# Optimization experiments

Measured on AMD Instinct MI355X. Metric: run time of the kernel, lower is better.

## Reference

```python
import jax, jax.numpy as jnp
import numpy as np
from jax import lax

D_MODEL, D_INNER, D_CONV, D_STATE, DT_RANK = 1024, 2048, 4, 16, 64
B, L = 2, 1024


def setup_inputs() -> dict:
    key = jax.random.key(0)
    ks = jax.random.split(key, 10)
    s = 0.02
    return {
        "x": jax.random.normal(ks[0], (B, L, D_MODEL), jnp.float32),
        "in_proj_w": jax.random.normal(ks[1], (2 * D_INNER, D_MODEL), jnp.float32) * s,
        "conv_w": jax.random.normal(ks[2], (D_INNER, 1, D_CONV), jnp.float32) * 0.1,
        "conv_b": jax.random.normal(ks[3], (D_INNER,), jnp.float32) * s,
        "x_proj_w": jax.random.normal(ks[4], (DT_RANK + 2 * D_STATE, D_INNER), jnp.float32) * s,
        "dt_proj_w": jax.random.normal(ks[5], (D_INNER, DT_RANK), jnp.float32) * s,
        "dt_proj_b": jax.random.normal(ks[6], (D_INNER,), jnp.float32) * s,
        "A_log": jnp.log(jnp.broadcast_to(jnp.arange(1, D_STATE + 1, dtype=jnp.float32), (D_INNER, D_STATE))),
        "D": jax.random.normal(ks[7], (D_INNER,), jnp.float32),
        "out_proj_w": jax.random.normal(ks[8], (D_MODEL, D_INNER), jnp.float32) * s,
    }


def _silu(v):
    return v * jax.nn.sigmoid(v)


def reference(x, in_proj_w, conv_w, conv_b, x_proj_w, dt_proj_w, dt_proj_b, A_log, D, out_proj_w):
    # in_proj: [B,L,d_model] -> [B,L,2*d_inner], split into x and gate z
    xz = jnp.einsum("bld,ed->ble", x, in_proj_w)
    xi, z = jnp.split(xz, 2, axis=-1)  # each [B,L,d_inner]

    # depthwise causal conv1d (padding = d_conv-1 on the left, output length L)
    xc = jnp.transpose(xi, (0, 2, 1))  # [B, d_inner, L]
    xc = lax.conv_general_dilated(
        xc, conv_w, window_strides=(1,), padding=[(D_CONV - 1, 0)],
        feature_group_count=D_INNER, dimension_numbers=("NCH", "OIH", "NCH"))
    xc = xc + conv_b[None, :, None]
    xc = _silu(jnp.transpose(xc, (0, 2, 1)))  # [B,L,d_inner]

    # selective scan parameters
    x_dbl = jnp.einsum("bld,ed->ble", xc, x_proj_w)  # [B,L,dt_rank+2*d_state]
    dt, Bm, Cm = jnp.split(x_dbl, [DT_RANK, DT_RANK + D_STATE], axis=-1)
    delta = jax.nn.softplus(jnp.einsum("blr,dr->bld", dt, dt_proj_w) + dt_proj_b)  # [B,L,d_inner]
    A = -jnp.exp(A_log)  # [d_inner, d_state]

    deltaA = jnp.exp(delta[..., None] * A)                       # [B,L,d_inner,N]
    deltaBu = delta[..., None] * Bm[:, :, None, :] * xc[..., None]  # [B,L,d_inner,N]

    def step(h, inp):
        a, bu, c = inp
        h = a * h + bu                         # [B,d_inner,N]
        y = jnp.einsum("bdn,bn->bd", h, c)     # [B,d_inner]
        return h, y

    h0 = jnp.zeros((x.shape[0], D_INNER, D_STATE), xc.dtype)
    _, ys = lax.scan(step, h0, (jnp.moveaxis(deltaA, 1, 0),
                                jnp.moveaxis(deltaBu, 1, 0),
                                jnp.moveaxis(Cm, 1, 0)))
    y = jnp.moveaxis(ys, 0, 1)  # [B,L,d_inner]

    y = y + xc * D
    y = y * _silu(z)
    return jnp.einsum("bld,ed->ble", y, out_proj_w)  # [B,L,d_model]
```

## Files before the change

kernel.cpp:

```cpp
#include <hip/hip_runtime.h>
#include <math.h>
#include <stdint.h>

#define DMODEL 1024
#define DINNER 2048
#define DCONV  4
#define DSTATE 16
#define DTRANK 64
#define BB 2
#define LL 1024
#define MM (BB * LL)

#define CL  64
#define NCH (LL / CL)

#define AS1(p) ((__attribute__((address_space(1))) void*)(void*)(p))
#define AS3(p) ((__attribute__((address_space(3))) void*)(void*)(p))

typedef __attribute__((ext_vector_type(8))) short bf16x8;
typedef __attribute__((ext_vector_type(4))) float f32x4;

__device__ __forceinline__ ushort bf16_rne(float f) {
  uint32_t u = __float_as_uint(f);
  uint32_t r = (u + 0x7fffu + ((u >> 16) & 1u)) >> 16;
  return (ushort)r;
}

__device__ __forceinline__ void split4(const float* __restrict__ in,
                                       ushort* __restrict__ hi,
                                       ushort* __restrict__ lo, int i4) {
  const float4 v = *reinterpret_cast<const float4*>(in + (size_t)i4 * 4);
  ushort4 h;
  h.x = bf16_rne(v.x); h.y = bf16_rne(v.y);
  h.z = bf16_rne(v.z); h.w = bf16_rne(v.w);
  *reinterpret_cast<ushort4*>(hi + (size_t)i4 * 4) = h;
  if (lo) {
    ushort4 l;
    l.x = bf16_rne(v.x - __uint_as_float((uint)h.x << 16));
    l.y = bf16_rne(v.y - __uint_as_float((uint)h.y << 16));
    l.z = bf16_rne(v.z - __uint_as_float((uint)h.z << 16));
    l.w = bf16_rne(v.w - __uint_as_float((uint)h.w << 16));
    *reinterpret_cast<ushort4*>(lo + (size_t)i4 * 4) = l;
  }
}

__global__ __launch_bounds__(256)
void split3(const float* s0, ushort* h0, ushort* l0, int n0,
            const float* s1, ushort* h1, ushort* l1, int n1,
            const float* s2, ushort* h2, ushort* l2, int n2,
            const float* s3, ushort* h3, ushort* l3, int n3) {
  int i = blockIdx.x * 256 + threadIdx.x;
  if (i < n0) { split4(s0, h0, l0, i); return; }
  i -= n0;
  if (i < n1) { split4(s1, h1, l1, i); return; }
  i -= n1;
  if (i < n2) { split4(s2, h2, l2, i); return; }
  i -= n2;
  if (i < n3) { split4(s3, h3, l3, i); return; }
}

__device__ __forceinline__ int swz4(int r) { return (r & 3) ^ ((r >> 2) & 3); }

template<int EPI, int SPLITK>
__global__ __launch_bounds__(256)
void gemm_hl_mfma(const ushort* __restrict__ Ahg, const ushort* __restrict__ Alg,
                  const ushort* __restrict__ Bhg, const ushort* __restrict__ Blg,
                  float* __restrict__ C, const float* __restrict__ bias,
                  int M, int N, int K) {
  __shared__ ushort Ah[2][128][32];
  __shared__ ushort Al[2][128][32];
  __shared__ ushort Bh[2][128][32];
  __shared__ ushort Bl[2][128][32];

  const int tid  = threadIdx.x;
  const int wave = tid >> 6;
  const int lane = tid & 63;
  const int m0 = blockIdx.y * 128;
  const int n0 = blockIdx.x * 128;
  const int wm = (wave >> 1) * 64;
  const int wn = (wave & 1) * 64;

  const int ksl = K / SPLITK;
  const int kb  = blockIdx.z * ksl;
  float* Cout   = C + (size_t)blockIdx.z * M * N;

  f32x4 acc[4][4];
  #pragma unroll
  for (int i = 0; i < 4; ++i)
    #pragma unroll
    for (int j = 0; j < 4; ++j)
      acc[i][j] = (f32x4){0.f, 0.f, 0.f, 0.f};

  const ushort* gsrc; ushort* dst; int row0;
  if      (wave == 0) { gsrc = Ahg; dst = &Ah[0][0][0]; row0 = m0; }
  else if (wave == 1) { gsrc = Alg; dst = &Al[0][0][0]; row0 = m0; }
  else if (wave == 2) { gsrc = Bhg; dst = &Bh[0][0][0]; row0 = n0; }
  else                { gsrc = Blg; dst = &Bl[0][0][0]; row0 = n0; }

  const int lr = lane >> 2;
  const int ls = lane & 3;
  const int fr = lane & 15;
  const int q  = lane >> 4;

  auto STAGE = [&](int bi, int k0) {
    ushort* d = dst + bi * 4096;
    #pragma unroll
    for (int seg = 0; seg < 8; ++seg) {
      const int rho = seg * 16 + lr;
      const int ks  = (ls ^ swz4(rho)) * 8;
      __builtin_amdgcn_global_load_lds(
          AS1(gsrc + (size_t)(row0 + rho) * K + k0 + ks),
          AS3(d + seg * 512), 16, 0, 0);
    }
  };

  const int NT = ksl / 32;
  STAGE(0, kb);
  __syncthreads();

  int cur = 0;
  for (int kt = 0; kt < NT; ++kt) {
    if (kt + 1 < NT) STAGE(cur ^ 1, kb + (kt + 1) * 32);

    bf16x8 ah[4], al[4], bh[4], bl[4];
    #pragma unroll
    for (int f = 0; f < 4; ++f) {
      { const int r = wm + f * 16 + fr; const int s = 8 * (q ^ swz4(r));
        ah[f] = *reinterpret_cast<const bf16x8*>(&Ah[cur][r][s]);
        al[f] = *reinterpret_cast<const bf16x8*>(&Al[cur][r][s]); }
      { const int r = wn + f * 16 + fr; const int s = 8 * (q ^ swz4(r));
        bh[f] = *reinterpret_cast<const bf16x8*>(&Bh[cur][r][s]);
        bl[f] = *reinterpret_cast<const bf16x8*>(&Bl[cur][r][s]); }
    }
    #pragma unroll
    for (int i = 0; i < 4; ++i)
      #pragma unroll
      for (int j = 0; j < 4; ++j) {
        acc[i][j] = __builtin_amdgcn_mfma_f32_16x16x32_bf16(ah[i], bh[j], acc[i][j], 0, 0, 0);
        acc[i][j] = __builtin_amdgcn_mfma_f32_16x16x32_bf16(al[i], bh[j], acc[i][j], 0, 0, 0);
        acc[i][j] = __builtin_amdgcn_mfma_f32_16x16x32_bf16(ah[i], bl[j], acc[i][j], 0, 0, 0);
      }

    __syncthreads();
    cur ^= 1;
  }

  const int cr = (lane >> 4) * 4;
  const int cc = lane & 15;
  #pragma unroll
  for (int i = 0; i < 4; ++i)
    #pragma unroll
    for (int j = 0; j < 4; ++j) {
      const int cn = n0 + wn + j * 16 + cc;
      const float bj = (EPI == 1) ? bias[cn] : 0.f;
      const size_t base = (size_t)(m0 + wm + i * 16 + cr) * N + cn;
      #pragma unroll
      for (int r = 0; r < 4; ++r) {
        float v = acc[i][j][r];
        if (EPI == 1) {
          v += bj;
          v = fmaxf(v, 0.f) + __logf(1.f + __expf(-fabsf(v)));
        }
        Cout[base + (size_t)r * N] = v;
      }
    }
}

template<int EPI, int SPLITK>
__global__ __launch_bounds__(256)
void gemm_p2_mfma(const ushort* __restrict__ Ahg, const ushort* __restrict__ Bhg,
                  const ushort* __restrict__ Blg, float* __restrict__ P,
                  int M, int N, int K) {
  __shared__ ushort Ah[2][128][32];
  __shared__ ushort Bh[2][128][32];
  __shared__ ushort Bl[2][128][32];

  const int tid  = threadIdx.x;
  const int wave = tid >> 6;
  const int lane = tid & 63;
  const int m0 = blockIdx.y * 128;
  const int n0 = blockIdx.x * 128;
  const int wm = (wave >> 1) * 64;
  const int wn = (wave & 1) * 64;

  const int ksl = K / SPLITK;
  const int kb  = blockIdx.z * ksl;
  float* Cout   = P + (size_t)blockIdx.z * M * N;

  f32x4 acc[4][4];
  #pragma unroll
  for (int i = 0; i < 4; ++i)
    #pragma unroll
    for (int j = 0; j < 4; ++j)
      acc[i][j] = (f32x4){0.f, 0.f, 0.f, 0.f};

  const ushort* gsrc = nullptr; ushort* dst = nullptr; int row0 = 0;
  if      (wave == 0) { gsrc = Ahg; dst = &Ah[0][0][0]; row0 = m0; }
  else if (wave == 1) { gsrc = Bhg; dst = &Bh[0][0][0]; row0 = n0; }
  else if (wave == 2) { gsrc = Blg; dst = &Bl[0][0][0]; row0 = n0; }

  const int lr = lane >> 2;
  const int ls = lane & 3;
  const int fr = lane & 15;
  const int q  = lane >> 4;

  auto STAGE = [&](int bi, int k0) {
    if (wave >= 3) return;
    ushort* d = dst + bi * 4096;
    #pragma unroll
    for (int seg = 0; seg < 8; ++seg) {
      const int rho = seg * 16 + lr;
      const int ks  = (ls ^ swz4(rho)) * 8;
      __builtin_amdgcn_global_load_lds(
          AS1(gsrc + (size_t)(row0 + rho) * K + k0 + ks),
          AS3(d + seg * 512), 16, 0, 0);
    }
  };

  const int NT = ksl / 32;
  STAGE(0, kb);
  __syncthreads();

  int cur = 0;
  for (int kt = 0; kt < NT; ++kt) {
    if (kt + 1 < NT) STAGE(cur ^ 1, kb + (kt + 1) * 32);

    bf16x8 ah[4], bh[4], bl[4];
    #pragma unroll
    for (int f = 0; f < 4; ++f) {
      { const int r = wm + f * 16 + fr; const int s = 8 * (q ^ swz4(r));
        ah[f] = *reinterpret_cast<const bf16x8*>(&Ah[cur][r][s]); }
      { const int r = wn + f * 16 + fr; const int s = 8 * (q ^ swz4(r));
        bh[f] = *reinterpret_cast<const bf16x8*>(&Bh[cur][r][s]);
        bl[f] = *reinterpret_cast<const bf16x8*>(&Bl[cur][r][s]); }
    }
    #pragma unroll
    for (int i = 0; i < 4; ++i)
      #pragma unroll
      for (int j = 0; j < 4; ++j) {
        acc[i][j] = __builtin_amdgcn_mfma_f32_16x16x32_bf16(ah[i], bh[j], acc[i][j], 0, 0, 0);
        acc[i][j] = __builtin_amdgcn_mfma_f32_16x16x32_bf16(ah[i], bl[j], acc[i][j], 0, 0, 0);
      }

    __syncthreads();
    cur ^= 1;
  }

  const int cr = (lane >> 4) * 4;
  const int cc = lane & 15;
  #pragma unroll
  for (int i = 0; i < 4; ++i)
    #pragma unroll
    for (int j = 0; j < 4; ++j) {
      const int cn = n0 + wn + j * 16 + cc;
      const size_t base = (size_t)(m0 + wm + i * 16 + cr) * N + cn;
      #pragma unroll
      for (int r = 0; r < 4; ++r) {
        float v = acc[i][j][r];
        if (EPI == 2 && cn >= DINNER)
          v = v / (1.f + __expf(-v));
        Cout[base + (size_t)r * N] = v;
      }
    }
}

__global__ __launch_bounds__(256)
void splitk_reduce4(const float* __restrict__ P, float* __restrict__ out, int n) {
  const int i = (blockIdx.x * 256 + threadIdx.x) * 4;
  if (i >= n) return;
  float4 s = *reinterpret_cast<const float4*>(P + i);
  #pragma unroll
  for (int z = 1; z < 4; ++z) {
    const float4 v = *reinterpret_cast<const float4*>(P + (size_t)z * n + i);
    s.x += v.x; s.y += v.y; s.z += v.z; s.w += v.w;
  }
  *reinterpret_cast<float4*>(out + i) = s;
}

template<int BM, int BN, int TM, int TN, int KSLICE>
__global__ __launch_bounds__(256)
void gemm_nt_part(const float* __restrict__ A, const float* __restrict__ Bw,
                  float* __restrict__ P, int M, int N, int lda, int ldb) {
  constexpr int BK  = 16;
  constexpr int NTX = BN / TN;
  constexpr int NTY = BM / TM;
  static_assert(NTX * NTY == 256, "thread tile mismatch");
  __shared__ float As[BK][BM + 4];
  __shared__ float Bs[BK][BN + 4];

  const int tid = threadIdx.x;
  const int m0  = blockIdx.y * BM;
  const int n0  = blockIdx.x * BN;
  const int kb  = blockIdx.z * KSLICE;
  const int tx  = tid % NTX;
  const int ty  = tid / NTX;

  float acc[TM][TN] = {};

  for (int k0 = kb; k0 < kb + KSLICE; k0 += BK) {
    __syncthreads();
    for (int t = tid; t < BM * 4; t += 256) {
      const int row = t >> 2, kq = t & 3;
      const float4 v = *reinterpret_cast<const float4*>(
          A + (size_t)(m0 + row) * lda + k0 + kq * 4);
      As[kq * 4 + 0][row] = v.x;
      As[kq * 4 + 1][row] = v.y;
      As[kq * 4 + 2][row] = v.z;
      As[kq * 4 + 3][row] = v.w;
    }
    for (int t = tid; t < BN * 4; t += 256) {
      const int row = t >> 2, kq = t & 3;
      const float4 v = *reinterpret_cast<const float4*>(
          Bw + (size_t)(n0 + row) * ldb + k0 + kq * 4);
      Bs[kq * 4 + 0][row] = v.x;
      Bs[kq * 4 + 1][row] = v.y;
      Bs[kq * 4 + 2][row] = v.z;
      Bs[kq * 4 + 3][row] = v.w;
    }
    __syncthreads();
    #pragma unroll
    for (int k = 0; k < BK; ++k) {
      float a[TM], b[TN];
      #pragma unroll
      for (int i = 0; i < TM; ++i) a[i] = As[k][ty * TM + i];
      #pragma unroll
      for (int j = 0; j < TN; ++j) b[j] = Bs[k][tx * TN + j];
      #pragma unroll
      for (int i = 0; i < TM; ++i)
        #pragma unroll
        for (int j = 0; j < TN; ++j)
          acc[i][j] = fmaf(a[i], b[j], acc[i][j]);
    }
  }

  float* out = P + (size_t)blockIdx.z * M * N;
  #pragma unroll
  for (int i = 0; i < TM; ++i)
    #pragma unroll
    for (int j = 0; j < TN; ++j)
      out[(size_t)(m0 + ty * TM + i) * N + n0 + tx * TN + j] = acc[i][j];
}

__global__ __launch_bounds__(256)
void xpr_fused(const float* __restrict__ part, float* __restrict__ xdbl,
               ushort* __restrict__ dth, ushort* __restrict__ dtl) {
  const int i = blockIdx.x * 256 + threadIdx.x;
  if (i >= MM * 24) return;
  const int m  = i / 24;
  const int c4 = (i % 24) * 4;
  const size_t off = (size_t)m * 96 + c4;
  float4 s = *reinterpret_cast<const float4*>(part + off);
  #pragma unroll
  for (int z = 1; z < 8; ++z) {
    const float4 v = *reinterpret_cast<const float4*>(part + (size_t)z * MM * 96 + off);
    s.x += v.x; s.y += v.y; s.z += v.z; s.w += v.w;
  }
  if (c4 < 64) {
    ushort4 h, l;
    h.x = bf16_rne(s.x); l.x = bf16_rne(s.x - __uint_as_float((uint)h.x << 16));
    h.y = bf16_rne(s.y); l.y = bf16_rne(s.y - __uint_as_float((uint)h.y << 16));
    h.z = bf16_rne(s.z); l.z = bf16_rne(s.z - __uint_as_float((uint)h.z << 16));
    h.w = bf16_rne(s.w); l.w = bf16_rne(s.w - __uint_as_float((uint)h.w << 16));
    *reinterpret_cast<ushort4*>(dth + (size_t)m * 64 + c4) = h;
    *reinterpret_cast<ushort4*>(dtl + (size_t)m * 64 + c4) = l;
  } else {
    *reinterpret_cast<float4*>(xdbl + off) = s;
  }
}

__global__ __launch_bounds__(256)
void conv_silu(const float* __restrict__ xz, const float* __restrict__ cw,
               const float* __restrict__ cb, float* __restrict__ xc) {
  const int idx = blockIdx.x * 256 + threadIdx.x;
  if (idx >= MM * DINNER / 4) return;
  const int d4 = (idx & 511) * 4;
  const int m  = idx >> 9;
  const int l  = m & (LL - 1);
  const int b  = m >> 10;

  float4 w0 = *reinterpret_cast<const float4*>(cw + (size_t)(d4 + 0) * 4);
  float4 w1 = *reinterpret_cast<const float4*>(cw + (size_t)(d4 + 1) * 4);
  float4 w2 = *reinterpret_cast<const float4*>(cw + (size_t)(d4 + 2) * 4);
  float4 w3 = *reinterpret_cast<const float4*>(cw + (size_t)(d4 + 3) * 4);
  float4 acc = *reinterpret_cast<const float4*>(cb + d4);

  #pragma unroll
  for (int j = 0; j < DCONV; ++j) {
    const int ll = l - (DCONV - 1) + j;
    if (ll >= 0) {
      const float4 xv = *reinterpret_cast<const float4*>(
          xz + ((size_t)(b * LL + ll) << 12) + d4);
      acc.x = fmaf(xv.x, (&w0.x)[j], acc.x);
      acc.y = fmaf(xv.y, (&w1.x)[j], acc.y);
      acc.z = fmaf(xv.z, (&w2.x)[j], acc.z);
      acc.w = fmaf(xv.w, (&w3.x)[j], acc.w);
    }
  }
  float4 o;
  o.x = acc.x / (1.f + __expf(-acc.x));
  o.y = acc.y / (1.f + __expf(-acc.y));
  o.z = acc.z / (1.f + __expf(-acc.z));
  o.w = acc.w / (1.f + __expf(-acc.w));
  *reinterpret_cast<float4*>(xc + (size_t)m * DINNER + d4) = o;
}

__device__ __forceinline__ void stage_tile(const float* g, int stride,
                                           float* ldst, int lane) {
  const int r  = lane >> 2;
  const int q4 = (lane & 3) * 4;
  #pragma unroll
  for (int i = 0; i < 4; ++i) {
    __builtin_amdgcn_global_load_lds(
        AS1(g + (size_t)(i * 16 + r) * stride + q4),
        AS3(ldst + i * 256), 16, 0, 0);
  }
}

__device__ __forceinline__ float quad_sum(float v) {
  int i = __float_as_int(v);
  v += __int_as_float(__builtin_amdgcn_update_dpp(0, i, 0xB1, 0xf, 0xf, true));
  i = __float_as_int(v);
  v += __int_as_float(__builtin_amdgcn_update_dpp(0, i, 0x4E, 0xf, 0xf, true));
  return v;
}

__global__ __launch_bounds__(64)
void scan_chunk_state(const float* __restrict__ delta, const float* __restrict__ xc,
                      const float* __restrict__ xdbl, const float* __restrict__ A_log,
                      float* __restrict__ hend, float* __restrict__ aprod) {
  __shared__ float dT[CL][16];
  __shared__ float xT[CL][16];
  __shared__ float bT[CL][16];

  const int idx = blockIdx.x;
  const int c  = idx & 15;
  const int dg = (idx >> 4) & 127;
  const int b  = idx >> 11;
  const int t  = threadIdx.x;
  const int ch = t >> 2;
  const int q  = t & 3;
  const int d  = dg * 16 + ch;

  const size_t r0 = (size_t)b * LL + (size_t)c * CL;
  stage_tile(delta + r0 * DINNER + dg * 16, DINNER, &dT[0][0], t);
  stage_tile(xc    + r0 * DINNER + dg * 16, DINNER, &xT[0][0], t);
  stage_tile(xdbl  + r0 * 96 + DTRANK,          96, &bT[0][0], t);

  float Adn[4];
  #pragma unroll
  for (int j = 0; j < 4; ++j)
    Adn[j] = -__expf(A_log[d * DSTATE + 4 * q + j]);
  float h0 = 0.f, h1 = 0.f, h2 = 0.f, h3 = 0.f;
  float p0 = 1.f, p1 = 1.f, p2 = 1.f, p3 = 1.f;

  __syncthreads();

  #pragma unroll 8
  for (int l = 0; l < CL; ++l) {
    const float dv = dT[l][ch];
    const float xv = xT[l][ch];
    const float4 B4 = *reinterpret_cast<const float4*>(&bT[l][4 * q]);
    const float dvx = dv * xv;
    const float a0 = __expf(dv * Adn[0]);
    const float a1 = __expf(dv * Adn[1]);
    const float a2 = __expf(dv * Adn[2]);
    const float a3 = __expf(dv * Adn[3]);
    h0 = fmaf(a0, h0, dvx * B4.x);  p0 *= a0;
    h1 = fmaf(a1, h1, dvx * B4.y);  p1 *= a1;
    h2 = fmaf(a2, h2, dvx * B4.z);  p2 *= a2;
    h3 = fmaf(a3, h3, dvx * B4.w);  p3 *= a3;
  }

  const size_t base = (((size_t)(b * NCH + c) * DINNER) + d) * DSTATE + 4 * q;
  *reinterpret_cast<float4*>(hend  + base) = (float4){h0, h1, h2, h3};
  *reinterpret_cast<float4*>(aprod + base) = (float4){p0, p1, p2, p3};
}

__global__ __launch_bounds__(256)
void scan_combine(const float* __restrict__ hend, const float* __restrict__ aprod,
                  float* __restrict__ hin) {
  const int tid = blockIdx.x * 256 + threadIdx.x;
  const size_t cstride = (size_t)DINNER * DSTATE;
  const size_t base = (size_t)(tid >> 15) * NCH * cstride + (tid & 32767);
  float h = 0.f;
  hin[base] = 0.f;
  #pragma unroll
  for (int c = 0; c < NCH - 1; ++c) {
    h = fmaf(aprod[base + (size_t)c * cstride], h, hend[base + (size_t)c * cstride]);
    hin[base + (size_t)(c + 1) * cstride] = h;
  }
}

__global__ __launch_bounds__(64)
void scan_apply(const float* __restrict__ delta, const float* __restrict__ xc,
                const float* __restrict__ xdbl, const float* __restrict__ xz,
                const float* __restrict__ A_log, const float* __restrict__ Dp,
                const float* __restrict__ hin, ushort* __restrict__ yh) {
  __shared__ float dT[CL][16];
  __shared__ float xT[CL][16];
  __shared__ float bT[CL][16];
  __shared__ float cT[CL][16];
  __shared__ float zT[CL][16];

  const int idx = blockIdx.x;
  const int c  = idx & 15;
  const int dg = (idx >> 4) & 127;
  const int b  = idx >> 11;
  const int t  = threadIdx.x;
  const int ch = t >> 2;
  const int q  = t & 3;
  const int d  = dg * 16 + ch;

  const size_t r0 = (size_t)b * LL + (size_t)c * CL;
  stage_tile(delta + r0 * DINNER + dg * 16, DINNER, &dT[0][0], t);
  stage_tile(xc    + r0 * DINNER + dg * 16, DINNER, &xT[0][0], t);
  stage_tile(xdbl  + r0 * 96 + DTRANK,          96, &bT[0][0], t);
  stage_tile(xdbl  + r0 * 96 + DTRANK + DSTATE, 96, &cT[0][0], t);
  stage_tile(xz    + (r0 << 12) + DINNER + dg * 16, 4096, &zT[0][0], t);

  float Adn[4];
  #pragma unroll
  for (int j = 0; j < 4; ++j)
    Adn[j] = -__expf(A_log[d * DSTATE + 4 * q + j]);
  const float Dd = Dp[d];

  const size_t base = (((size_t)(b * NCH + c) * DINNER) + d) * DSTATE + 4 * q;
  const float4 h4 = *reinterpret_cast<const float4*>(hin + base);
  float h0 = h4.x, h1 = h4.y, h2 = h4.z, h3 = h4.w;

  __syncthreads();

  #pragma unroll 8
  for (int l = 0; l < CL; ++l) {
    const float dv = dT[l][ch];
    const float xv = xT[l][ch];
    const float4 B4 = *reinterpret_cast<const float4*>(&bT[l][4 * q]);
    const float4 C4 = *reinterpret_cast<const float4*>(&cT[l][4 * q]);
    const float dvx = dv * xv;
    const float a0 = __expf(dv * Adn[0]);
    const float a1 = __expf(dv * Adn[1]);
    const float a2 = __expf(dv * Adn[2]);
    const float a3 = __expf(dv * Adn[3]);
    h0 = fmaf(a0, h0, dvx * B4.x);
    h1 = fmaf(a1, h1, dvx * B4.y);
    h2 = fmaf(a2, h2, dvx * B4.z);
    h3 = fmaf(a3, h3, dvx * B4.w);
    float ys = fmaf(h0, C4.x, fmaf(h1, C4.y, fmaf(h2, C4.z, h3 * C4.w)));
    ys = quad_sum(ys);
    if (q == 0) {
      const float g = zT[l][ch];
      const float tv = (ys + xv * Dd) * g;
      yh[(r0 + l) * (size_t)DINNER + d] = bf16_rne(tv);
    }
  }
}

extern "C" void kernel_launch(void* const* d_in, const int* in_sizes, int n_in,
                              void* d_out, int out_size, void* d_ws, size_t ws_size,
                              hipStream_t stream) {
  const float* x         = (const float*)d_in[0];
  const float* in_proj_w = (const float*)d_in[1];
  const float* conv_w    = (const float*)d_in[2];
  const float* conv_b    = (const float*)d_in[3];
  const float* x_proj_w  = (const float*)d_in[4];
  const float* dt_proj_w = (const float*)d_in[5];
  const float* dt_proj_b = (const float*)d_in[6];
  const float* A_log     = (const float*)d_in[7];
  const float* Dv        = (const float*)d_in[8];
  const float* out_proj_w= (const float*)d_in[9];
  float* out = (float*)d_out;

  float* ws    = (float*)d_ws;
  float* xz    = ws;
  float* xc    = xz    + (size_t)MM * 4096;
  float* xdbl  = xc    + (size_t)MM * DINNER;
  float* delta = xdbl  + (size_t)MM * 96;
  ushort* us   = (ushort*)(delta + (size_t)MM * DINNER);
  ushort* yhp  = us;
  ushort* ylp  = yhp + (size_t)MM * DINNER;
  ushort* xh   = ylp + (size_t)MM * DINNER;
  ushort* xl   = xh  + (size_t)MM * DMODEL;
  ushort* wih  = xl  + (size_t)MM * DMODEL;
  ushort* wil  = wih + (size_t)4096 * DMODEL;
  ushort* woh  = wil + (size_t)4096 * DMODEL;
  ushort* wol  = woh + (size_t)DMODEL * DINNER;

  ushort* dth = ylp;
  ushort* dtl = ylp + 131072;
  ushort* wdh = ylp + 262144;
  ushort* wdl = ylp + 393216;

  float* hend  = (float*)wih;
  float* aprod = hend  + (size_t)BB * NCH * DINNER * DSTATE;
  float* hin   = aprod + (size_t)BB * NCH * DINNER * DSTATE;
  float* part  = hend;
  float* opart = xz;

  const dim3 blk(256);

  {
    const int n0 = (MM * DMODEL) / 4, n1 = (4096 * DMODEL) / 4,
              n2 = (DMODEL * DINNER) / 4, n3 = (DINNER * DTRANK) / 4;
    split3<<<dim3((n0 + n1 + n2 + n3) / 256), blk, 0, stream>>>(
        x, xh, nullptr, n0, in_proj_w, wih, wil, n1,
        out_proj_w, woh, wol, n2, dt_proj_w, wdh, wdl, n3);
  }

  gemm_p2_mfma<2,1><<<dim3(4096 / 128, MM / 128), blk, 0, stream>>>(
      xh, wih, wil, xz, MM, 4096, DMODEL);

  conv_silu<<<dim3((MM * DINNER / 4) / 256), blk, 0, stream>>>(xz, conv_w, conv_b, xc);

  gemm_nt_part<64,32,4,2,256><<<dim3(96/32, MM/64, 8), blk, 0, stream>>>(
      xc, x_proj_w, part, MM, 96, DINNER, DINNER);
  xpr_fused<<<dim3((MM * 24 + 255) / 256), blk, 0, stream>>>(part, xdbl, dth, dtl);

  gemm_hl_mfma<1,1><<<dim3(DINNER / 128, MM / 128), blk, 0, stream>>>(
      dth, dtl, wdh, wdl, delta, dt_proj_b, MM, DINNER, DTRANK);

  scan_chunk_state<<<dim3(BB * 128 * NCH), dim3(64), 0, stream>>>(
      delta, xc, xdbl, A_log, hend, aprod);
  scan_combine<<<dim3(BB * DINNER * DSTATE / 256), blk, 0, stream>>>(
      hend, aprod, hin);
  scan_apply<<<dim3(BB * 128 * NCH), dim3(64), 0, stream>>>(
      delta, xc, xdbl, xz, A_log, Dv, hin, yhp);

  gemm_p2_mfma<0,4><<<dim3(DMODEL / 128, MM / 128, 4), blk, 0, stream>>>(
      yhp, woh, wol, opart, MM, DMODEL, DINNER);
  splitk_reduce4<<<dim3((MM * DMODEL) / 1024), blk, 0, stream>>>(
      opart, out, MM * DMODEL);
}
```

Before: 183.1 us.

## Load GEMM A operand directly to registers and drop lo-split for out_proj

Unifies the three MFMA GEMM kernels into one templated kernel that stages only the B (weight) operand through LDS and loads A fragments directly from global memory into registers, prefetching the next tile. All four waves now share the B staging work. The out_proj GEMM also drops the low bf16 correction term of its weights (NB=1), halving its MFMA count and weight traffic. This cuts LDS footprint and traffic, but A loads become uncoalesced 16-byte global reads per lane. Dropping the weight low part lowers out_proj precision.

Measured after the change: 198.6 us. +8.5%, slower.

```diff
diff --git a/kernel.cpp b/kernel.cpp
--- a/kernel.cpp
+++ b/kernel.cpp
@@ -61,16 +61,13 @@
 
 __device__ __forceinline__ int swz4(int r) { return (r & 3) ^ ((r >> 2) & 3); }
 
-template<int EPI, int SPLITK>
-__global__ __launch_bounds__(256)
-void gemm_hl_mfma(const ushort* __restrict__ Ahg, const ushort* __restrict__ Alg,
+template<int NB, bool ALO, int EPI, int SPLITK>
+__global__ __launch_bounds__(256)
+void gemm_adirect(const ushort* __restrict__ Ag, const ushort* __restrict__ Alg,
                   const ushort* __restrict__ Bhg, const ushort* __restrict__ Blg,
                   float* __restrict__ C, const float* __restrict__ bias,
                   int M, int N, int K) {
-  __shared__ ushort Ah[2][128][32];
-  __shared__ ushort Al[2][128][32];
-  __shared__ ushort Bh[2][128][32];
-  __shared__ ushort Bl[2][128][32];
+  __shared__ ushort Bst[NB * 2][128][32];
 
   const int tid  = threadIdx.x;
   const int wave = tid >> 6;
@@ -91,57 +88,75 @@
     for (int j = 0; j < 4; ++j)
       acc[i][j] = (f32x4){0.f, 0.f, 0.f, 0.f};
 
-  const ushort* gsrc; ushort* dst; int row0;
-  if      (wave == 0) { gsrc = Ahg; dst = &Ah[0][0][0]; row0 = m0; }
-  else if (wave == 1) { gsrc = Alg; dst = &Al[0][0][0]; row0 = m0; }
-  else if (wave == 2) { gsrc = Bhg; dst = &Bh[0][0][0]; row0 = n0; }
-  else                { gsrc = Blg; dst = &Bl[0][0][0]; row0 = n0; }
-
   const int lr = lane >> 2;
   const int ls = lane & 3;
   const int fr = lane & 15;
   const int q  = lane >> 4;
 
   auto STAGE = [&](int bi, int k0) {
-    ushort* d = dst + bi * 4096;
-    #pragma unroll
-    for (int seg = 0; seg < 8; ++seg) {
+    #pragma unroll
+    for (int j = 0; j < NB * 2; ++j) {
+      const int g   = wave * NB * 2 + j;
+      const int p   = g >> 3;
+      const int seg = g & 7;
+      const ushort* src = p ? Blg : Bhg;
       const int rho = seg * 16 + lr;
       const int ks  = (ls ^ swz4(rho)) * 8;
       __builtin_amdgcn_global_load_lds(
-          AS1(gsrc + (size_t)(row0 + rho) * K + k0 + ks),
-          AS3(d + seg * 512), 16, 0, 0);
+          AS1(src + (size_t)(n0 + rho) * K + k0 + ks),
+          AS3(&Bst[p * 2 + bi][0][0] + seg * 512), 16, 0, 0);
     }
   };
 
+  auto LOADA = [&](bf16x8* dh, bf16x8* dl, int kt) {
+    #pragma unroll
+    for (int f = 0; f < 4; ++f) {
+      const size_t off = (size_t)(m0 + wm + f * 16 + fr) * K + kb + kt * 32 + q * 8;
+      dh[f] = *reinterpret_cast<const bf16x8*>(Ag + off);
+      if constexpr (ALO)
+        dl[f] = *reinterpret_cast<const bf16x8*>(Alg + off);
+    }
+  };
+
   const int NT = ksl / 32;
+  bf16x8 ahc[4], alc[4], ahn[4], aln[4];
   STAGE(0, kb);
+  LOADA(ahc, alc, 0);
   __syncthreads();
 
   int cur = 0;
   for (int kt = 0; kt < NT; ++kt) {
-    if (kt + 1 < NT) STAGE(cur ^ 1, kb + (kt + 1) * 32);
-
-    bf16x8 ah[4], al[4], bh[4], bl[4];
+    if (kt + 1 < NT) {
+      STAGE(cur ^ 1, kb + (kt + 1) * 32);
+      LOADA(ahn, aln, kt + 1);
+    }
+
+    bf16x8 bh[4], bl[4];
     #pragma unroll
     for (int f = 0; f < 4; ++f) {
-      { const int r = wm + f * 16 + fr; const int s = 8 * (q ^ swz4(r));
-        ah[f] = *reinterpret_cast<const bf16x8*>(&Ah[cur][r][s]);
-        al[f] = *reinterpret_cast<const bf16x8*>(&Al[cur][r][s]); }
-      { const int r = wn + f * 16 + fr; const int s = 8 * (q ^ swz4(r));
-        bh[f] = *reinterpret_cast<const bf16x8*>(&Bh[cur][r][s]);
-        bl[f] = *reinterpret_cast<const bf16x8*>(&Bl[cur][r][s]); }
+      const int r = wn + f * 16 + fr;
+      const int s = 8 * (q ^ swz4(r));
+      bh[f] = *reinterpret_cast<const bf16x8*>(&Bst[cur][r][s]);
+      if (NB == 2)
+        bl[f] = *reinterpret_cast<const bf16x8*>(&Bst[2 + cur][r][s]);
     }
     #pragma unroll
     for (int i = 0; i < 4; ++i)
       #pragma unroll
       for (int j = 0; j < 4; ++j) {
-        acc[i][j] = __builtin_amdgcn_mfma_f32_16x16x32_bf16(ah[i], bh[j], acc[i][j], 0, 0, 0);
-        acc[i][j] = __builtin_amdgcn_mfma_f32_16x16x32_bf16(al[i], bh[j], acc[i][j], 0, 0, 0);
-        acc[i][j] = __builtin_amdgcn_mfma_f32_16x16x32_bf16(ah[i], bl[j], acc[i][j], 0, 0, 0);
+        acc[i][j] = __builtin_amdgcn_mfma_f32_16x16x32_bf16(ahc[i], bh[j], acc[i][j], 0, 0, 0);
+        if (NB == 2)
+          acc[i][j] = __builtin_amdgcn_mfma_f32_16x16x32_bf16(ahc[i], bl[j], acc[i][j], 0, 0, 0);
+        if constexpr (ALO)
+          acc[i][j] = __builtin_amdgcn_mfma_f32_16x16x32_bf16(alc[i], bh[j], acc[i][j], 0, 0, 0);
       }
 
     __syncthreads();
+    #pragma unroll
+    for (int f = 0; f < 4; ++f) {
+      ahc[f] = ahn[f];
+      if constexpr (ALO) alc[f] = aln[f];
+    }
     cur ^= 1;
   }
 
@@ -161,102 +176,6 @@
           v += bj;
           v = fmaxf(v, 0.f) + __logf(1.f + __expf(-fabsf(v)));
         }
-        Cout[base + (size_t)r * N] = v;
-      }
-    }
-}
-
-template<int EPI, int SPLITK>
-__global__ __launch_bounds__(256)
-void gemm_p2_mfma(const ushort* __restrict__ Ahg, const ushort* __restrict__ Bhg,
-                  const ushort* __restrict__ Blg, float* __restrict__ P,
-                  int M, int N, int K) {
-  __shared__ ushort Ah[2][128][32];
-  __shared__ ushort Bh[2][128][32];
-  __shared__ ushort Bl[2][128][32];
-
-  const int tid  = threadIdx.x;
-  const int wave = tid >> 6;
-  const int lane = tid & 63;
-  const int m0 = blockIdx.y * 128;
-  const int n0 = blockIdx.x * 128;
-  const int wm = (wave >> 1) * 64;
-  const int wn = (wave & 1) * 64;
-
-  const int ksl = K / SPLITK;
-  const int kb  = blockIdx.z * ksl;
-  float* Cout   = P + (size_t)blockIdx.z * M * N;
-
-  f32x4 acc[4][4];
-  #pragma unroll
-  for (int i = 0; i < 4; ++i)
-    #pragma unroll
-    for (int j = 0; j < 4; ++j)
-      acc[i][j] = (f32x4){0.f, 0.f, 0.f, 0.f};
-
-  const ushort* gsrc = nullptr; ushort* dst = nullptr; int row0 = 0;
-  if      (wave == 0) { gsrc = Ahg; dst = &Ah[0][0][0]; row0 = m0; }
-  else if (wave == 1) { gsrc = Bhg; dst = &Bh[0][0][0]; row0 = n0; }
-  else if (wave == 2) { gsrc = Blg; dst = &Bl[0][0][0]; row0 = n0; }
-
-  const int lr = lane >> 2;
-  const int ls = lane & 3;
-  const int fr = lane & 15;
-  const int q  = lane >> 4;
-
-  auto STAGE = [&](int bi, int k0) {
-    if (wave >= 3) return;
-    ushort* d = dst + bi * 4096;
-    #pragma unroll
-    for (int seg = 0; seg < 8; ++seg) {
-      const int rho = seg * 16 + lr;
-      const int ks  = (ls ^ swz4(rho)) * 8;
-      __builtin_amdgcn_global_load_lds(
-          AS1(gsrc + (size_t)(row0 + rho) * K + k0 + ks),
-          AS3(d + seg * 512), 16, 0, 0);
-    }
-  };
-
-  const int NT = ksl / 32;
-  STAGE(0, kb);
-  __syncthreads();
-
-  int cur = 0;
-  for (int kt = 0; kt < NT; ++kt) {
-    if (kt + 1 < NT) STAGE(cur ^ 1, kb + (kt + 1) * 32);
-
-    bf16x8 ah[4], bh[4], bl[4];
-    #pragma unroll
-    for (int f = 0; f < 4; ++f) {
-      { const int r = wm + f * 16 + fr; const int s = 8 * (q ^ swz4(r));
-        ah[f] = *reinterpret_cast<const bf16x8*>(&Ah[cur][r][s]); }
-      { const int r = wn + f * 16 + fr; const int s = 8 * (q ^ swz4(r));
-        bh[f] = *reinterpret_cast<const bf16x8*>(&Bh[cur][r][s]);
-        bl[f] = *reinterpret_cast<const bf16x8*>(&Bl[cur][r][s]); }
-    }
-    #pragma unroll
-    for (int i = 0; i < 4; ++i)
-      #pragma unroll
-      for (int j = 0; j < 4; ++j) {
-        acc[i][j] = __builtin_amdgcn_mfma_f32_16x16x32_bf16(ah[i], bh[j], acc[i][j], 0, 0, 0);
-        acc[i][j] = __builtin_amdgcn_mfma_f32_16x16x32_bf16(ah[i], bl[j], acc[i][j], 0, 0, 0);
-      }
-
-    __syncthreads();
-    cur ^= 1;
-  }
-
-  const int cr = (lane >> 4) * 4;
-  const int cc = lane & 15;
-  #pragma unroll
-  for (int i = 0; i < 4; ++i)
-    #pragma unroll
-    for (int j = 0; j < 4; ++j) {
-      const int cn = n0 + wn + j * 16 + cc;
-      const size_t base = (size_t)(m0 + wm + i * 16 + cr) * N + cn;
-      #pragma unroll
-      for (int r = 0; r < 4; ++r) {
-        float v = acc[i][j][r];
         if (EPI == 2 && cn >= DINNER)
           v = v / (1.f + __expf(-v));
         Cout[base + (size_t)r * N] = v;
@@ -603,11 +522,11 @@
               n2 = (DMODEL * DINNER) / 4, n3 = (DINNER * DTRANK) / 4;
     split3<<<dim3((n0 + n1 + n2 + n3) / 256), blk, 0, stream>>>(
         x, xh, nullptr, n0, in_proj_w, wih, wil, n1,
-        out_proj_w, woh, wol, n2, dt_proj_w, wdh, wdl, n3);
-  }
-
-  gemm_p2_mfma<2,1><<<dim3(4096 / 128, MM / 128), blk, 0, stream>>>(
-      xh, wih, wil, xz, MM, 4096, DMODEL);
+        out_proj_w, woh, nullptr, n2, dt_proj_w, wdh, wdl, n3);
+  }
+
+  gemm_adirect<2, false, 2, 1><<<dim3(4096 / 128, MM / 128), blk, 0, stream>>>(
+      xh, nullptr, wih, wil, xz, nullptr, MM, 4096, DMODEL);
 
   conv_silu<<<dim3((MM * DINNER / 4) / 256), blk, 0, stream>>>(xz, conv_w, conv_b, xc);
 
@@ -615,7 +534,7 @@
       xc, x_proj_w, part, MM, 96, DINNER, DINNER);
   xpr_fused<<<dim3((MM * 24 + 255) / 256), blk, 0, stream>>>(part, xdbl, dth, dtl);
 
-  gemm_hl_mfma<1,1><<<dim3(DINNER / 128, MM / 128), blk, 0, stream>>>(
+  gemm_adirect<2, true, 1, 1><<<dim3(DINNER / 128, MM / 128), blk, 0, stream>>>(
       dth, dtl, wdh, wdl, delta, dt_proj_b, MM, DINNER, DTRANK);
 
   scan_chunk_state<<<dim3(BB * 128 * NCH), dim3(64), 0, stream>>>(
@@ -625,8 +544,8 @@
   scan_apply<<<dim3(BB * 128 * NCH), dim3(64), 0, stream>>>(
       delta, xc, xdbl, xz, A_log, Dv, hin, yhp);
 
-  gemm_p2_mfma<0,4><<<dim3(DMODEL / 128, MM / 128, 4), blk, 0, stream>>>(
-      yhp, woh, wol, opart, MM, DMODEL, DINNER);
+  gemm_adirect<1, false, 0, 4><<<dim3(DMODEL / 128, MM / 128, 4), blk, 0, stream>>>(
+      yhp, nullptr, woh, nullptr, opart, nullptr, MM, DMODEL, DINNER);
   splitk_reduce4<<<dim3((MM * DMODEL) / 1024), blk, 0, stream>>>(
       opart, out, MM * DMODEL);
 }
```
